# Optimization experiments

Hardware: AMD Instinct MI355X
Metric: run time of the kernel (lower is better)

Reference implementation:

```python
import jax, jax.numpy as jnp
import numpy as np

EMBED_DIM = 1024
NUM_HEADS = 16
HEAD_DIM = EMBED_DIM // NUM_HEADS


def setup_inputs() -> dict:
    key = jax.random.key(0)
    ks = jax.random.split(key, 9)
    B, S, E = 2, 2048, EMBED_DIM
    scale = 1.0 / np.sqrt(E)
    inp = {
        "x": jax.random.normal(ks[0], (B, S, E), dtype=jnp.float32),
        "Wq": jax.random.normal(ks[1], (E, E), dtype=jnp.float32) * scale,
        "bq": jnp.zeros((E,), dtype=jnp.float32),
        "Wk": jax.random.normal(ks[2], (E, E), dtype=jnp.float32) * scale,
        "bk": jnp.zeros((E,), dtype=jnp.float32),
        "Wv": jax.random.normal(ks[3], (E, E), dtype=jnp.float32) * scale,
        "bv": jnp.zeros((E,), dtype=jnp.float32),
        "Wo": jax.random.normal(ks[4], (E, E), dtype=jnp.float32) * scale,
        "bo": jnp.zeros((E,), dtype=jnp.float32),
    }
    return inp


def reference(x, Wq, bq, Wk, bk, Wv, bv, Wo, bo):
    B, S, E = x.shape
    H, D = NUM_HEADS, HEAD_DIM
    sm_scale = D ** (-0.5)

    def proj(W, b):
        # torch Linear: x @ W.T + b ; reshape to [B, H, S, D]
        y = jnp.einsum("bse,fe->bsf", x, W) + b
        return y.reshape(B, S, H, D).transpose(0, 2, 1, 3)

    q = proj(Wq, bq)  # [B, H, S, D]
    k = proj(Wk, bk)
    v = proj(Wv, bv)

    scores = jnp.einsum("bhqd,bhkd->bhqk", q, k) * sm_scale  # [B, H, S, S]
    attn = jax.nn.softmax(scores, axis=-1)
    o = jnp.einsum("bhqk,bhkd->bhqd", attn, v)  # [B, H, S, D]
    o = o.transpose(0, 2, 1, 3).reshape(B, S, E)
    return jnp.einsum("bse,fe->bsf", o, Wo) + bo
```

## Files before the change

kernel.cpp:

```cpp
#include <hip/hip_runtime.h>
#include <hip/hip_fp16.h>
#include <stdint.h>


typedef _Float16 f16;
typedef _Float16 f16x8 __attribute__((ext_vector_type(8)));
typedef _Float16 f16x4v __attribute__((ext_vector_type(4)));
typedef _Float16 f16x2 __attribute__((ext_vector_type(2)));
typedef float f32x4 __attribute__((ext_vector_type(4)));

#define BQ  2
#define SEQ 2048
#define EMB 1024
#define NH  16
#define HD  64
#define MM  (BQ * SEQ)

__device__ __forceinline__ void gld_lds16(const void* g, void* l) {
  __builtin_amdgcn_global_load_lds(
      (const __attribute__((address_space(1))) void*)g,
      (__attribute__((address_space(3))) void*)l, 16, 0, 0);
}

__device__ __forceinline__ void stage128x64(const f16* __restrict__ src,
                                            int ld, f16* lds, int tid) {
#pragma unroll
  for (int it = 0; it < 4; ++it) {
    int idx = it * 256 + tid;
    int r = idx >> 3, c = idx & 7;
    int sc = c ^ (r & 7);
    gld_lds16(src + (size_t)r * ld + sc * 8, lds + idx * 8);
  }
}

__global__ void cvt4(const float* __restrict__ src, f16* __restrict__ dst,
                     int n4) {
  int i = blockIdx.x * blockDim.x + threadIdx.x;
  if (i < n4) {
    float4 v = ((const float4*)src)[i];
    f16x4v o;
    o[0] = (f16)v.x; o[1] = (f16)v.y; o[2] = (f16)v.z; o[3] = (f16)v.w;
    ((f16x4v*)dst)[i] = o;
  }
}

__global__ void cvtW4(const float* __restrict__ s0, const float* __restrict__ s1,
                      const float* __restrict__ s2, const float* __restrict__ s3,
                      f16* __restrict__ d0, f16* __restrict__ d1,
                      f16* __restrict__ d2, f16* __restrict__ d3, int n4) {
  int i = blockIdx.x * blockDim.x + threadIdx.x;
  if (i >= n4) return;
  const float* s = (blockIdx.y == 0) ? s0 : (blockIdx.y == 1) ? s1
                   : (blockIdx.y == 2) ? s2 : s3;
  f16* d = (blockIdx.y == 0) ? d0 : (blockIdx.y == 1) ? d1
           : (blockIdx.y == 2) ? d2 : d3;
  float4 v = ((const float4*)s)[i];
  f16x4v o;
  o[0] = (f16)v.x; o[1] = (f16)v.y; o[2] = (f16)v.z; o[3] = (f16)v.w;
  ((f16x4v*)d)[i] = o;
}

template <int MODE>
__global__ __launch_bounds__(256, 2) void gemm_bt(
    const f16* __restrict__ A, const f16* __restrict__ W0,
    const f16* __restrict__ W1, const f16* __restrict__ W2,
    const float* __restrict__ b0, const float* __restrict__ b1,
    const float* __restrict__ b2, f16* __restrict__ o0, f16* __restrict__ o1,
    f16* __restrict__ o2, float* __restrict__ fo) {
  __shared__ __align__(16) f16 As[128 * 64];
  __shared__ __align__(16) f16 Bs[128 * 64];

  const int tid = threadIdx.x, lane = tid & 63, wid = tid >> 6;
  const int z = blockIdx.z;
  const f16* W = (z == 0) ? W0 : (z == 1 ? W1 : W2);
  const float* bia = (z == 0) ? b0 : (z == 1 ? b1 : b2);
  f16* outp = (z == 0) ? o0 : (z == 1 ? o1 : o2);
  const int row0 = blockIdx.x * 128, col0 = blockIdx.y * 128;
  const int wr = (wid >> 1) * 64, wc = (wid & 1) * 64;
  const int rb = lane & 15, gq = lane >> 4, sw = lane & 7;

  f32x4 acc[4][4] = {};

  for (int kt = 0; kt < EMB / 64; ++kt) {
    __syncthreads();
    stage128x64(A + (size_t)row0 * EMB + kt * 64, EMB, As, tid);
    stage128x64(W + (size_t)col0 * EMB + kt * 64, EMB, Bs, tid);
    asm volatile("s_waitcnt vmcnt(0)" ::: "memory");
    __syncthreads();
#pragma unroll
    for (int kk = 0; kk < 2; ++kk) {
      f16x8 av[4], bv[4];
#pragma unroll
      for (int f = 0; f < 4; ++f) {
        av[f] = *(const f16x8*)(As + (wr + f * 16 + rb) * 64 +
                                (((kk * 4 + gq) ^ sw) << 3));
        bv[f] = *(const f16x8*)(Bs + (wc + f * 16 + rb) * 64 +
                                (((kk * 4 + gq) ^ sw) << 3));
      }
#pragma unroll
      for (int fi = 0; fi < 4; ++fi)
#pragma unroll
        for (int fj = 0; fj < 4; ++fj)
          acc[fi][fj] = __builtin_amdgcn_mfma_f32_16x16x32_f16(
              av[fi], bv[fj], acc[fi][fj], 0, 0, 0);
    }
  }

  float bias[4];
#pragma unroll
  for (int fj = 0; fj < 4; ++fj) bias[fj] = bia[col0 + wc + fj * 16 + rb];
  const float scale = (MODE == 0 && z == 0) ? 0.18033688011112042f : 1.0f;
#pragma unroll
  for (int fi = 0; fi < 4; ++fi) {
#pragma unroll
    for (int i = 0; i < 4; ++i) {
      int row = row0 + wr + fi * 16 + gq * 4 + i;
#pragma unroll
      for (int fj = 0; fj < 4; ++fj) {
        int col = col0 + wc + fj * 16 + rb;
        float v = (acc[fi][fj][i] + bias[fj]) * scale;
        if (MODE == 0) {
          int bb = row >> 11, s = row & (SEQ - 1);
          int h = col >> 6, d = col & 63;
          outp[(((size_t)(bb * NH + h)) * SEQ + s) * HD + d] = (f16)v;
        } else {
          fo[(size_t)row * EMB + col] = v;
        }
      }
    }
  }
}

__global__ __launch_bounds__(256) void vtrans(const f16* __restrict__ V,
                                              f16* __restrict__ Vt) {
  __shared__ f16 T[64][72];
  const int tid = threadIdx.x;
  const int s0 = blockIdx.x * 64, bh = blockIdx.y;
  const f16* Vh = V + (size_t)bh * SEQ * HD;
  f16* Vth = Vt + (size_t)bh * HD * SEQ;
#pragma unroll
  for (int it = 0; it < 2; ++it) {
    int idx = it * 256 + tid;
    int r = idx >> 3, c0 = (idx & 7) * 8;
    *(f16x8*)&T[r][c0] = *(const f16x8*)(Vh + (size_t)(s0 + r) * HD + c0);
  }
  __syncthreads();
#pragma unroll
  for (int it = 0; it < 2; ++it) {
    int idx = it * 256 + tid;
    int d = idx >> 3, sc = (idx & 7) * 8;
    f16x8 v;
#pragma unroll
    for (int j = 0; j < 8; ++j) v[j] = T[sc + j][d];
    *(f16x8*)(Vth + (size_t)d * SEQ + s0 + sc) = v;
  }
}

__global__ __launch_bounds__(256, 2) void attn_fwd(const f16* __restrict__ Q,
                                                   const f16* __restrict__ K,
                                                   const f16* __restrict__ Vt,
                                                   f16* __restrict__ O) {
  __shared__ __align__(16) f16 Ks[4][64 * 64];
  __shared__ __align__(16) f16 Vs[4][64 * 64];
  __shared__ __align__(16) f16 Ps[4][32 * 64];

  const int tid = threadIdx.x, lane = tid & 63, wid = tid >> 6;
  const int orig = blockIdx.x;
  const int swz = ((orig & 7) << 6) + (orig >> 3);
  const int qt = swz & 15, bh = swz >> 4;
  const f16* Qh = Q + (size_t)bh * SEQ * HD;
  const f16* Kh = K + (size_t)bh * SEQ * HD;
  const f16* Vth = Vt + (size_t)bh * HD * SEQ;
  const int q0 = qt * 128 + wid * 32;
  const int rb = lane & 15, gq = lane >> 4, sw = lane & 7;

  f16x8 aq[2][2];
#pragma unroll
  for (int qf = 0; qf < 2; ++qf)
#pragma unroll
    for (int kk = 0; kk < 2; ++kk)
      aq[qf][kk] = *(const f16x8*)(Qh + (size_t)(q0 + qf * 16 + rb) * HD +
                                   kk * 32 + gq * 8);
  asm volatile("s_waitcnt vmcnt(0)" ::: "memory");

  const int srow = tid >> 3, scol = (tid & 7) ^ (srow & 7);
  const f16* Kg0 = Kh + (size_t)srow * HD + scol * 8;
  const f16* Vg0 = Vth + (size_t)srow * SEQ + scol * 8;

  const int NT = SEQ / 64;
#pragma unroll
  for (int p = 0; p < 3; ++p) {
    const f16* kg = Kg0 + (size_t)p * 64 * HD;
    const f16* vg = Vg0 + p * 64;
    gld_lds16(kg,            &Ks[p][tid * 8]);
    gld_lds16(kg + 32 * HD,  &Ks[p][(tid + 256) * 8]);
    gld_lds16(vg,            &Vs[p][tid * 8]);
    gld_lds16(vg + 32 * SEQ, &Vs[p][(tid + 256) * 8]);
  }

  f16* Pw = &Ps[wid][0];
  f16* pwr[2][4];
#pragma unroll
  for (int qf = 0; qf < 2; ++qf)
#pragma unroll
    for (int cf = 0; cf < 4; ++cf)
      pwr[qf][cf] = Pw + (qf * 16 + rb) * 64 +
                    (((2 * cf + (gq >> 1)) ^ sw) << 3) + ((gq & 1) << 2);

  f16x8 ones;
#pragma unroll
  for (int j = 0; j < 8; ++j) ones[j] = (f16)1.0f;

  f32x4 oacc[2][4] = {};
  f32x4 lacc[2] = {};

  for (int t = 0; t < NT; ++t) {
    __builtin_amdgcn_s_barrier();
    __builtin_amdgcn_sched_barrier(0);
    {
      const int tp = (t + 3 < NT) ? t + 3 : NT - 1;
      f16* Kn = &Ks[(t + 3) & 3][0];
      f16* Vn = &Vs[(t + 3) & 3][0];
      const f16* kg = Kg0 + (size_t)tp * 64 * HD;
      const f16* vg = Vg0 + tp * 64;
      gld_lds16(kg,            Kn + tid * 8);
      gld_lds16(kg + 32 * HD,  Kn + (tid + 256) * 8);
      gld_lds16(vg,            Vn + tid * 8);
      gld_lds16(vg + 32 * SEQ, Vn + (tid + 256) * 8);
      asm volatile("s_waitcnt vmcnt(12)" ::: "memory");
    }
    __builtin_amdgcn_s_barrier();
    __builtin_amdgcn_sched_barrier(0);

    const f16* Kb = &Ks[t & 3][0];
    const f16* Vb = &Vs[t & 3][0];

    f32x4 s_[2][4] = {};
#pragma unroll
    for (int kk = 0; kk < 2; ++kk) {
      f16x8 bk[4];
#pragma unroll
      for (int cf = 0; cf < 4; ++cf)
        bk[cf] = *(const f16x8*)(Kb + (cf * 16 + rb) * 64 +
                                 (((kk * 4 + gq) ^ sw) << 3));
#pragma unroll
      for (int qf = 0; qf < 2; ++qf)
#pragma unroll
        for (int cf = 0; cf < 4; ++cf)
          s_[qf][cf] = __builtin_amdgcn_mfma_f32_16x16x32_f16(
              bk[cf], aq[qf][kk], s_[qf][cf], 0, 0, 0);
    }

#pragma unroll
    for (int qf = 0; qf < 2; ++qf)
#pragma unroll
      for (int cf = 0; cf < 4; ++cf) {
        float e0 = __builtin_amdgcn_exp2f(s_[qf][cf][0]);
        float e1 = __builtin_amdgcn_exp2f(s_[qf][cf][1]);
        float e2 = __builtin_amdgcn_exp2f(s_[qf][cf][2]);
        float e3 = __builtin_amdgcn_exp2f(s_[qf][cf][3]);
        f16x2 h01 = __builtin_bit_cast(f16x2, __builtin_amdgcn_cvt_pkrtz(e0, e1));
        f16x2 h23 = __builtin_bit_cast(f16x2, __builtin_amdgcn_cvt_pkrtz(e2, e3));
        f16x4v w;
        w[0] = h01[0]; w[1] = h01[1]; w[2] = h23[0]; w[3] = h23[1];
        *(f16x4v*)pwr[qf][cf] = w;
      }

#pragma unroll
    for (int kk = 0; kk < 2; ++kk) {
      f16x8 pa[2];
#pragma unroll
      for (int qf = 0; qf < 2; ++qf)
        pa[qf] = *(const f16x8*)(Pw + (qf * 16 + rb) * 64 +
                                 (((kk * 4 + gq) ^ sw) << 3));
      lacc[0] = __builtin_amdgcn_mfma_f32_16x16x32_f16(pa[0], ones, lacc[0], 0, 0, 0);
      lacc[1] = __builtin_amdgcn_mfma_f32_16x16x32_f16(pa[1], ones, lacc[1], 0, 0, 0);
#pragma unroll
      for (int df = 0; df < 4; ++df) {
        f16x8 vb = *(const f16x8*)(Vb + (df * 16 + rb) * 64 +
                                   (((kk * 4 + gq) ^ sw) << 3));
        oacc[0][df] = __builtin_amdgcn_mfma_f32_16x16x32_f16(pa[0], vb, oacc[0][df], 0, 0, 0);
        oacc[1][df] = __builtin_amdgcn_mfma_f32_16x16x32_f16(pa[1], vb, oacc[1][df], 0, 0, 0);
      }
    }
  }
  asm volatile("s_waitcnt vmcnt(0)" ::: "memory");

  const int b = bh >> 4, h = bh & 15;
#pragma unroll
  for (int qf = 0; qf < 2; ++qf)
#pragma unroll
    for (int i = 0; i < 4; ++i) {
      const float inv = 1.0f / lacc[qf][i];
      const int s = q0 + qf * 16 + gq * 4 + i;
      f16* orow = O + ((size_t)(b * SEQ + s)) * EMB + h * 64 + rb;
#pragma unroll
      for (int df = 0; df < 4; ++df)
        orow[df * 16] = (f16)(oacc[qf][df][i] * inv);
    }
}

extern "C" void kernel_launch(void* const* d_in, const int* in_sizes, int n_in,
                              void* d_out, int out_size, void* d_ws,
                              size_t ws_size, hipStream_t stream) {
  const float* x = (const float*)d_in[0];
  const float* Wq = (const float*)d_in[1];
  const float* bq = (const float*)d_in[2];
  const float* Wk = (const float*)d_in[3];
  const float* bk = (const float*)d_in[4];
  const float* Wv = (const float*)d_in[5];
  const float* bv = (const float*)d_in[6];
  const float* Wo = (const float*)d_in[7];
  const float* bo = (const float*)d_in[8];
  float* out = (float*)d_out;

  const size_t NX = (size_t)MM * EMB;
  const size_t NW = (size_t)EMB * EMB;

  f16* xh  = (f16*)d_ws;
  f16* wqh = xh + NX;
  f16* wkh = wqh + NW;
  f16* wvh = wkh + NW;
  f16* woh = wvh + NW;
  f16* Qw  = woh + NW;
  f16* Kw  = Qw + NX;
  f16* Vw  = Kw + NX;
  f16* Vtw = Vw + NX;
  f16* Ow  = Vtw + NX;

  cvt4<<<(int)(NX / 4 / 256), 256, 0, stream>>>(x, xh, (int)(NX / 4));
  cvtW4<<<dim3((int)(NW / 4 / 256), 4), 256, 0, stream>>>(
      Wq, Wk, Wv, Wo, wqh, wkh, wvh, woh, (int)(NW / 4));

  gemm_bt<0><<<dim3(MM / 128, EMB / 128, 3), 256, 0, stream>>>(
      xh, wqh, wkh, wvh, bq, bk, bv, Qw, Kw, Vw, nullptr);

  vtrans<<<dim3(SEQ / 64, BQ * NH), 256, 0, stream>>>(Vw, Vtw);

  attn_fwd<<<dim3(512), 256, 0, stream>>>(Qw, Kw, Vtw, Ow);

  gemm_bt<1><<<dim3(MM / 128, EMB / 128, 1), 256, 0, stream>>>(
      Ow, woh, woh, woh, bo, bo, bo, nullptr, nullptr, nullptr, out);
}
```

Baseline: 113.0 us.

## Keep softmax probabilities in registers and feed PV via 16x16x16 MFMA

The exponentiated scores no longer make a round trip through shared memory. The QK^T output fragments are reused directly as A operands of 16x16x16 MFMAs, with V reads re-indexed so the operands line up. This frees the P buffer in LDS. The K/V ring is also cut from four stages to three, which lets launch bounds go up to 3 blocks per CU. The trade-off is twice as many smaller MFMA instructions, more V LDS reads, a shallower prefetch depth, and tighter register pressure at higher occupancy.

```diff
diff --git a/kernel.cpp b/kernel.cpp
--- a/kernel.cpp
+++ b/kernel.cpp
@@ -6,7 +6,7 @@
 typedef _Float16 f16;
 typedef _Float16 f16x8 __attribute__((ext_vector_type(8)));
 typedef _Float16 f16x4v __attribute__((ext_vector_type(4)));
-typedef _Float16 f16x2 __attribute__((ext_vector_type(2)));
+typedef __fp16 hf4 __attribute__((ext_vector_type(4)));
 typedef float f32x4 __attribute__((ext_vector_type(4)));
 
 #define BQ  2
@@ -156,13 +156,12 @@
   }
 }
 
-__global__ __launch_bounds__(256, 2) void attn_fwd(const f16* __restrict__ Q,
+__global__ __launch_bounds__(256, 3) void attn_fwd(const f16* __restrict__ Q,
                                                    const f16* __restrict__ K,
                                                    const f16* __restrict__ Vt,
                                                    f16* __restrict__ O) {
-  __shared__ __align__(16) f16 Ks[4][64 * 64];
-  __shared__ __align__(16) f16 Vs[4][64 * 64];
-  __shared__ __align__(16) f16 Ps[4][32 * 64];
+  __shared__ __align__(16) f16 Ks[3][64 * 64];
+  __shared__ __align__(16) f16 Vs[3][64 * 64];
 
   const int tid = threadIdx.x, lane = tid & 63, wid = tid >> 6;
   const int orig = blockIdx.x;
@@ -189,7 +188,7 @@
 
   const int NT = SEQ / 64;
 #pragma unroll
-  for (int p = 0; p < 3; ++p) {
+  for (int p = 0; p < 2; ++p) {
     const f16* kg = Kg0 + (size_t)p * 64 * HD;
     const f16* vg = Vg0 + p * 64;
     gld_lds16(kg,            &Ks[p][tid * 8]);
@@ -198,18 +197,14 @@
     gld_lds16(vg + 32 * SEQ, &Vs[p][(tid + 256) * 8]);
   }
 
-  f16* Pw = &Ps[wid][0];
-  f16* pwr[2][4];
-#pragma unroll
-  for (int qf = 0; qf < 2; ++qf)
-#pragma unroll
-    for (int cf = 0; cf < 4; ++cf)
-      pwr[qf][cf] = Pw + (qf * 16 + rb) * 64 +
-                    (((2 * cf + (gq >> 1)) ^ sw) << 3) + ((gq & 1) << 2);
-
-  f16x8 ones;
-#pragma unroll
-  for (int j = 0; j < 8; ++j) ones[j] = (f16)1.0f;
+  int voffb[4];
+#pragma unroll
+  for (int cf = 0; cf < 4; ++cf)
+    voffb[cf] = rb * 64 + (((2 * cf + (gq >> 1)) ^ sw) << 3) + ((gq & 1) << 2);
+
+  hf4 onesv;
+#pragma unroll
+  for (int j = 0; j < 4; ++j) onesv[j] = (__fp16)1.0f;
 
   f32x4 oacc[2][4] = {};
   f32x4 lacc[2] = {};
@@ -218,22 +213,22 @@
     __builtin_amdgcn_s_barrier();
     __builtin_amdgcn_sched_barrier(0);
     {
-      const int tp = (t + 3 < NT) ? t + 3 : NT - 1;
-      f16* Kn = &Ks[(t + 3) & 3][0];
-      f16* Vn = &Vs[(t + 3) & 3][0];
+      const int tp = (t + 2 < NT) ? t + 2 : NT - 1;
+      f16* Kn = &Ks[(t + 2) % 3][0];
+      f16* Vn = &Vs[(t + 2) % 3][0];
       const f16* kg = Kg0 + (size_t)tp * 64 * HD;
       const f16* vg = Vg0 + tp * 64;
       gld_lds16(kg,            Kn + tid * 8);
       gld_lds16(kg + 32 * HD,  Kn + (tid + 256) * 8);
       gld_lds16(vg,            Vn + tid * 8);
       gld_lds16(vg + 32 * SEQ, Vn + (tid + 256) * 8);
-      asm volatile("s_waitcnt vmcnt(12)" ::: "memory");
+      asm volatile("s_waitcnt vmcnt(8)" ::: "memory");
     }
     __builtin_amdgcn_s_barrier();
     __builtin_amdgcn_sched_barrier(0);
 
-    const f16* Kb = &Ks[t & 3][0];
-    const f16* Vb = &Vs[t & 3][0];
+    const f16* Kb = &Ks[t % 3][0];
+    const f16* Vb = &Vs[t % 3][0];
 
     f32x4 s_[2][4] = {};
 #pragma unroll
@@ -251,6 +246,7 @@
               bk[cf], aq[qf][kk], s_[qf][cf], 0, 0, 0);
     }
 
+    hf4 pa[2][4];
 #pragma unroll
     for (int qf = 0; qf < 2; ++qf)
 #pragma unroll
@@ -259,28 +255,27 @@
         float e1 = __builtin_amdgcn_exp2f(s_[qf][cf][1]);
         float e2 = __builtin_amdgcn_exp2f(s_[qf][cf][2]);
         float e3 = __builtin_amdgcn_exp2f(s_[qf][cf][3]);
-        f16x2 h01 = __builtin_bit_cast(f16x2, __builtin_amdgcn_cvt_pkrtz(e0, e1));
-        f16x2 h23 = __builtin_bit_cast(f16x2, __builtin_amdgcn_cvt_pkrtz(e2, e3));
-        f16x4v w;
+        auto h01 = __builtin_amdgcn_cvt_pkrtz(e0, e1);
+        auto h23 = __builtin_amdgcn_cvt_pkrtz(e2, e3);
+        hf4 w;
         w[0] = h01[0]; w[1] = h01[1]; w[2] = h23[0]; w[3] = h23[1];
-        *(f16x4v*)pwr[qf][cf] = w;
+        pa[qf][cf] = w;
       }
 
 #pragma unroll
-    for (int kk = 0; kk < 2; ++kk) {
-      f16x8 pa[2];
-#pragma unroll
-      for (int qf = 0; qf < 2; ++qf)
-        pa[qf] = *(const f16x8*)(Pw + (qf * 16 + rb) * 64 +
-                                 (((kk * 4 + gq) ^ sw) << 3));
-      lacc[0] = __builtin_amdgcn_mfma_f32_16x16x32_f16(pa[0], ones, lacc[0], 0, 0, 0);
-      lacc[1] = __builtin_amdgcn_mfma_f32_16x16x32_f16(pa[1], ones, lacc[1], 0, 0, 0);
-#pragma unroll
-      for (int df = 0; df < 4; ++df) {
-        f16x8 vb = *(const f16x8*)(Vb + (df * 16 + rb) * 64 +
-                                   (((kk * 4 + gq) ^ sw) << 3));
-        oacc[0][df] = __builtin_amdgcn_mfma_f32_16x16x32_f16(pa[0], vb, oacc[0][df], 0, 0, 0);
-        oacc[1][df] = __builtin_amdgcn_mfma_f32_16x16x32_f16(pa[1], vb, oacc[1][df], 0, 0, 0);
+    for (int cf = 0; cf < 4; ++cf) {
+      hf4 vb[4];
+#pragma unroll
+      for (int df = 0; df < 4; ++df)
+        vb[df] = *(const hf4*)(Vb + voffb[cf] + df * 1024);
+#pragma unroll
+      for (int qf = 0; qf < 2; ++qf) {
+        lacc[qf] = __builtin_amdgcn_mfma_f32_16x16x16f16(pa[qf][cf], onesv,
+                                                         lacc[qf], 0, 0, 0);
+#pragma unroll
+        for (int df = 0; df < 4; ++df)
+          oacc[qf][df] = __builtin_amdgcn_mfma_f32_16x16x16f16(
+              pa[qf][cf], vb[df], oacc[qf][df], 0, 0, 0);
       }
     }
   }
```

After: 114.4 us. Within noise of the previous version (+1.3%).
